# Optimization experiments

Hardware: AMD Instinct MI355X
Metric: run time of the kernel (lower is better)

## Reference

```python
import jax, jax.numpy as jnp
import numpy as np

PRE_NMS_TOPK = 6000
POST_NMS_TOPK = 1000
NMS_THRESH = 0.7
MIN_SIZE = 16.0
NEG = -1e9  # stand-in for -inf that is safe under autodiff


def setup_inputs() -> dict:
    key = jax.random.key(0)
    k1, k2, k3, k4, k5, k6, k7, k8 = jax.random.split(key, 8)
    B, A = 8, 200000
    N = B * A
    # realistic anchors: centers within a ~1333x800 canvas, sizes 16..256
    cx = jax.random.uniform(k1, (N,), minval=0.0, maxval=1200.0)
    cy = jax.random.uniform(k2, (N,), minval=0.0, maxval=800.0)
    w = jax.random.uniform(k3, (N,), minval=16.0, maxval=256.0)
    h = jax.random.uniform(k4, (N,), minval=16.0, maxval=256.0)
    anchors = jnp.stack([cx - 0.5 * w, cy - 0.5 * h, cx + 0.5 * w, cy + 0.5 * h], axis=1)
    batch_indices = jnp.sort(jax.random.randint(k5, (N,), 0, B)).astype(jnp.int32)
    image_sizes = jax.random.randint(k6, (B, 2), 600, 1334).astype(jnp.int32)  # (H, W)
    objectness_logits = jax.random.normal(k7, (N, 1), dtype=jnp.float32)
    bbox_deltas = jax.random.normal(k8, (N, 4), dtype=jnp.float32) * 0.2
    return {
        'anchors': anchors,
        'batch_indices': batch_indices,
        'image_sizes': image_sizes,
        'objectness_logits': objectness_logits,
        'bbox_deltas': bbox_deltas,
    }


def _nms_one(bx, sc):
    """Greedy NMS on [K,4] boxes / [K] scores; returns POST_NMS_TOPK (idx, ok)."""
    K = bx.shape[0]
    areas = (bx[:, 2] - bx[:, 0]) * (bx[:, 3] - bx[:, 1])
    ar = jnp.arange(K)

    def step(sup, _):
        s = jnp.where(sup, NEG, sc)
        j = jnp.argmax(s)
        ok = s[j] > 0.5 * NEG
        b = bx[j]
        ix1 = jnp.maximum(b[0], bx[:, 0])
        iy1 = jnp.maximum(b[1], bx[:, 1])
        ix2 = jnp.minimum(b[2], bx[:, 2])
        iy2 = jnp.minimum(b[3], bx[:, 3])
        inter = jnp.maximum(ix2 - ix1, 0.0) * jnp.maximum(iy2 - iy1, 0.0)
        iou = inter / (areas + areas[j] - inter + 1e-9)
        sup = sup | (iou > NMS_THRESH) | (ar == j)
        return sup, (j, ok)

    sup0 = sc <= 0.5 * NEG  # padded / invalid entries start suppressed
    _, (idx, ok) = jax.lax.scan(step, sup0, None, length=POST_NMS_TOPK)
    return idx, ok


def reference(anchors, batch_indices, image_sizes, objectness_logits, bbox_deltas):
    B = image_sizes.shape[0]
    N = anchors.shape[0]
    sizes = image_sizes[batch_indices].astype(jnp.float32)  # [N,2] (H,W) per anchor

    # --- box decode ---
    a_w = anchors[:, 2] - anchors[:, 0]
    a_h = anchors[:, 3] - anchors[:, 1]
    a_x = anchors[:, 0] + 0.5 * a_w
    a_y = anchors[:, 1] + 0.5 * a_h
    t_x, t_y = bbox_deltas[:, 0], bbox_deltas[:, 1]
    t_w, t_h = bbox_deltas[:, 2], bbox_deltas[:, 3]
    p_x = a_x + t_x * a_w
    p_y = a_y + t_y * a_h
    p_w = a_w * jnp.exp(jnp.clip(t_w, -10.0, 10.0))
    p_h = a_h * jnp.exp(jnp.clip(t_h, -10.0, 10.0))
    x1 = p_x - 0.5 * p_w
    y1 = p_y - 0.5 * p_h
    x2 = p_x + 0.5 * p_w
    y2 = p_y + 0.5 * p_h

    # --- clip to image ---
    H, W = sizes[:, 0], sizes[:, 1]
    x1 = jnp.clip(x1, 0.0, W - 1.0)
    y1 = jnp.clip(y1, 0.0, H - 1.0)
    x2 = jnp.clip(x2, 0.0, W - 1.0)
    y2 = jnp.clip(y2, 0.0, H - 1.0)
    boxes = jnp.stack([x1, y1, x2, y2], axis=1)  # [N,4]

    # --- min-size filter (as score masking) ---
    valid = ((x2 - x1) >= MIN_SIZE) & ((y2 - y1) >= MIN_SIZE)
    fg = jax.nn.sigmoid(objectness_logits[:, 0])

    # --- per-image top-k over masked scores ---
    img_mask = batch_indices[None, :] == jnp.arange(B, dtype=batch_indices.dtype)[:, None]  # [B,N]
    scores = jnp.where(img_mask & valid[None, :], fg[None, :], NEG)  # [B,N]
    top_scores, top_idx = jax.lax.top_k(scores, PRE_NMS_TOPK)  # [B,PRE]
    top_boxes = boxes[top_idx]  # [B,PRE,4]

    # --- NMS per image ---
    keep_idx, keep_ok = jax.vmap(_nms_one)(top_boxes, top_scores)  # [B,POST]

    sel = jnp.take_along_axis(top_idx, keep_idx, axis=1)  # global anchor indices [B,POST]
    okf = keep_ok[..., None].astype(boxes.dtype)
    props = jnp.take_along_axis(top_boxes, keep_idx[..., None], axis=1) * okf  # [B,POST,4]
    obj = objectness_logits[sel] * okf  # [B,POST,1]
    deltas_out = bbox_deltas[sel] * okf  # [B,POST,4]
    bidx = jnp.where(keep_ok, jnp.arange(B, dtype=jnp.int32)[:, None], -1)  # [B,POST]

    return (props.reshape(-1, 4), bidx.reshape(-1), obj.reshape(-1, 1),
            deltas_out.reshape(-1, 4), keep_ok.reshape(-1))
```

## Files before the change

kernel.cpp:

```cpp
#include <hip/hip_runtime.h>
#include <stdint.h>

#define PRE_K   6000
#define POST_K  1000
#define CAP     8192
#define BINS    1024
#define ROWS    6016
#define CH      94
#define JSPLIT  8
#define NEGF    -1000000000.0f
#define IOU_EPS 16.0f
#define KREG    12


__device__ __forceinline__ uint32_t orderf(float f) {
  uint32_t u = __float_as_uint(f);
  return (u & 0x80000000u) ? ~u : (u | 0x80000000u);
}

__device__ __forceinline__ int score_bin(float sc) {
  int bin = (int)floorf((sc + 12.0f) * ((float)BINS / 24.0f));
  return bin < 0 ? 0 : (bin > BINS - 1 ? BINS - 1 : bin);
}

__device__ __forceinline__ int bin_slot(int bin) {
  return ((bin & 15) << 6) | (bin >> 4);
}

__device__ __forceinline__ void wg_barrier_lds() {
  asm volatile("s_waitcnt lgkmcnt(0)" ::: "memory");
  __builtin_amdgcn_s_barrier();
  asm volatile("" ::: "memory");
}

__device__ __forceinline__ void decode_box(
    const float* __restrict__ anchors, const float* __restrict__ deltas,
    const int* __restrict__ isz, int n, int b,
    double& x1, double& y1, double& x2, double& y2, bool& valid) {
  double ax1 = (double)anchors[4 * n + 0], ay1 = (double)anchors[4 * n + 1];
  double ax2 = (double)anchors[4 * n + 2], ay2 = (double)anchors[4 * n + 3];
  double aw = ax2 - ax1, ah = ay2 - ay1;
  double acx = ax1 + 0.5 * aw, acy = ay1 + 0.5 * ah;
  double tx = (double)deltas[4 * n + 0], ty = (double)deltas[4 * n + 1];
  double tw = (double)deltas[4 * n + 2], th = (double)deltas[4 * n + 3];
  tw = tw < -10.0 ? -10.0 : (tw > 10.0 ? 10.0 : tw);
  th = th < -10.0 ? -10.0 : (th > 10.0 ? 10.0 : th);
  double px = acx + tx * aw, py = acy + ty * ah;
  double pw = aw * exp(tw), ph = ah * exp(th);
  double H = (double)isz[2 * b + 0], W = (double)isz[2 * b + 1];
  double wm = W - 1.0, hm = H - 1.0;
  x1 = px - 0.5 * pw; y1 = py - 0.5 * ph;
  x2 = px + 0.5 * pw; y2 = py + 0.5 * ph;
  x1 = fmin(fmax(x1, 0.0), wm); x2 = fmin(fmax(x2, 0.0), wm);
  y1 = fmin(fmax(y1, 0.0), hm); y2 = fmin(fmax(y2, 0.0), hm);
  valid = (x2 - x1 >= 16.0) && (y2 - y1 >= 16.0);
}

__device__ __forceinline__ bool iou_exact(const double* __restrict__ tbox,
                                          const double* __restrict__ tarea,
                                          size_t ri, size_t ci) {
  const double* pr = &tbox[ri * 4];
  const double* pc = &tbox[ci * 4];
  double w = fmin(pr[2], pc[2]) - fmax(pr[0], pc[0]); w = w > 0.0 ? w : 0.0;
  double h = fmin(pr[3], pc[3]) - fmax(pr[1], pc[1]); h = h > 0.0 ? h : 0.0;
  double it = w * h;
  return it > 0.7 * (tarea[ri] + tarea[ci] - it + 1e-9);
}


__global__ void __launch_bounds__(256) k_score(const float* __restrict__ anchors,
                                               const int* __restrict__ bix,
                                               const int* __restrict__ isz,
                                               const float* __restrict__ logits,
                                               const float* __restrict__ deltas,
                                               float* __restrict__ scores,
                                               uint32_t* __restrict__ hist, int N) {
  const int SPAN = 4096;
  int start = blockIdx.x * SPAN;
  int end = start + SPAN < N ? start + SPAN : N;
  __shared__ uint32_t lh[2][BINS];
  for (int i = threadIdx.x; i < 2 * BINS; i += 256) ((uint32_t*)lh)[i] = 0u;
  __shared__ int s_b0, s_b1;
  if (threadIdx.x == 0) { s_b0 = bix[start]; s_b1 = bix[end - 1]; }
  __syncthreads();
  int b0 = s_b0, b1 = s_b1;

  for (int n = start + (int)threadIdx.x; n < end; n += 256) {
    int b = bix[n];
    double x1, y1, x2, y2; bool valid;
    decode_box(anchors, deltas, isz, n, b, x1, y1, x2, y2, valid);
    float sc = valid ? logits[n] : NEGF;
    scores[n] = sc;
    if (valid) {
      int bin = score_bin(sc);
      if (b == b0)      atomicAdd(&lh[0][bin], 1u);
      else if (b == b1) atomicAdd(&lh[1][bin], 1u);
      else              atomicAdd(&hist[b * BINS + bin_slot(bin)], 1u);
    }
  }
  __syncthreads();
  for (int bin = threadIdx.x; bin < BINS; bin += 256) {
    uint32_t c0 = lh[0][bin];
    if (c0) atomicAdd(&hist[b0 * BINS + bin_slot(bin)], c0);
    if (b1 != b0) {
      uint32_t c1 = lh[1][bin];
      if (c1) atomicAdd(&hist[b1 * BINS + bin_slot(bin)], c1);
    }
  }
}

__global__ void __launch_bounds__(1024) k_compact(const float* __restrict__ scores,
                                                  const int* __restrict__ bix,
                                                  const uint32_t* __restrict__ hist,
                                                  uint32_t* __restrict__ cnt,
                                                  uint64_t* __restrict__ cand, int N) {
  const int SPAN = 8192;
  int start = blockIdx.x * SPAN;
  int end = start + SPAN < N ? start + SPAN : N;
  int t = threadIdx.x;
  __shared__ int s_b0, s_b1;
  __shared__ uint32_t sh[BINS];
  __shared__ int s_bs;
  __shared__ uint32_t lcnt[8], lbase[8];
  if (t == 0) { s_b0 = bix[start]; s_b1 = bix[end - 1]; }
  if (t < 8) lcnt[t] = 0u;
  __syncthreads();
  int b0 = s_b0, b1 = s_b1;

  uint32_t bs0 = 0, bs1 = 0;
  for (int pass = 0; pass < 2; pass++) {
    int b = pass == 0 ? b0 : b1;
    if (pass == 1 && b1 == b0) { bs1 = bs0; break; }
    if (t < BINS) sh[t] = hist[b * BINS + bin_slot(t)];
    if (t == 0) s_bs = 0;
    __syncthreads();
    for (int off = 1; off < BINS; off <<= 1) {
      uint32_t v = (t < BINS && t + off < BINS) ? sh[t + off] : 0u;
      __syncthreads();
      if (t < BINS) sh[t] += v;
      __syncthreads();
    }
    if (t < BINS && sh[t] >= PRE_K) atomicMax(&s_bs, t);
    __syncthreads();
    if (pass == 0) bs0 = (uint32_t)s_bs; else bs1 = (uint32_t)s_bs;
    __syncthreads();
  }

  bool     predv[8];
  uint64_t keyv[8];
  uint32_t lposv[8];
  int      bv[8];
  int nt = 0;
  for (int base = start; base < end; base += 1024, nt++) {
    int n = base + t;
    bool pred = false; int b = 0; uint64_t key = 0ull; uint32_t lp = 0u;
    if (n < end) {
      float sc = scores[n];
      if (sc > 0.5f * NEGF) {
        b = bix[n];
        uint32_t bs = (b == b0) ? bs0 : bs1;
        if ((uint32_t)score_bin(sc) >= bs) {
          pred = true;
          key = ((uint64_t)orderf(sc) << 32) | (uint64_t)(uint32_t)(~(uint32_t)n);
          lp = atomicAdd(&lcnt[b], 1u);
        }
      }
    }
    predv[nt] = pred; keyv[nt] = key; lposv[nt] = lp; bv[nt] = b;
  }
  __syncthreads();
  if (t < 8) {
    uint32_t c = lcnt[t];
    lbase[t] = c ? atomicAdd(&cnt[t], c) : 0u;
  }
  __syncthreads();
  for (int k = 0; k < nt; k++) {
    if (predv[k]) {
      uint32_t pos = lbase[bv[k]] + lposv[k];
      if (pos < CAP) cand[(size_t)bv[k] * CAP + pos] = keyv[k];
    }
  }
}

__global__ void __launch_bounds__(256) k_rank(const uint64_t* __restrict__ cand,
                                              const uint32_t* __restrict__ cnt,
                                              uint32_t* __restrict__ prank) {
  int blk = blockIdx.x;
  int js = blk % JSPLIT;
  int ic = (blk / JSPLIT) % 32;
  int b  = blk / (JSPLIT * 32);
  int t = threadIdx.x;
  int C = (int)min(cnt[b], (uint32_t)CAP);
  if (ic * 256 >= C) return;
  const uint64_t* g = cand + (size_t)b * CAP;
  int i = ic * 256 + t;
  uint64_t ki = (i < C) ? g[i] : 0ull;

  int q = (C + JSPLIT - 1) / JSPLIT;
  int j0 = js * q;
  int j1 = j0 + q < C ? j0 + q : C;

  __shared__ uint64_t tile[1024];
  int rank = 0;
  for (int base = j0; base < j1; base += 1024) {
#pragma unroll
    for (int u = 0; u < 4; u++) {
      int j = base + u * 256 + t;
      tile[u * 256 + t] = (j < j1) ? g[j] : 0ull;
    }
    __syncthreads();
    int lim = j1 - base < 1024 ? j1 - base : 1024;
    const ulonglong2* t2 = (const ulonglong2*)tile;
    int pairs = lim >> 1;
    int jj = 0;
    for (; jj + 4 <= pairs; jj += 4) {
      ulonglong2 v0 = t2[jj + 0], v1 = t2[jj + 1];
      ulonglong2 v2 = t2[jj + 2], v3 = t2[jj + 3];
      rank += (v0.x > ki) ? 1 : 0; rank += (v0.y > ki) ? 1 : 0;
      rank += (v1.x > ki) ? 1 : 0; rank += (v1.y > ki) ? 1 : 0;
      rank += (v2.x > ki) ? 1 : 0; rank += (v2.y > ki) ? 1 : 0;
      rank += (v3.x > ki) ? 1 : 0; rank += (v3.y > ki) ? 1 : 0;
    }
    for (; jj < pairs; jj++) {
      ulonglong2 v = t2[jj];
      rank += (v.x > ki) ? 1 : 0; rank += (v.y > ki) ? 1 : 0;
    }
    if (lim & 1) rank += (tile[lim - 1] > ki) ? 1 : 0;
    __syncthreads();
  }
  if (i < C) prank[((size_t)b * JSPLIT + js) * CAP + i] = (uint32_t)rank;
}

__global__ void __launch_bounds__(256) k_place_gather(
    const uint64_t* __restrict__ cand, const uint32_t* __restrict__ cnt,
    const uint32_t* __restrict__ prank,
    const float* __restrict__ anchors, const float* __restrict__ deltas,
    const int* __restrict__ isz,
    double* __restrict__ tbox, double* __restrict__ tarea,
    float4* __restrict__ tboxf, float* __restrict__ tareaf,
    int* __restrict__ top_n, int* __restrict__ Cnum, int B) {
  int idx = blockIdx.x * blockDim.x + threadIdx.x;
  if (idx >= B * CAP) return;
  int b = idx / CAP, i = idx % CAP;
  int C = (int)min(cnt[b], (uint32_t)CAP);
  if (i == 0) Cnum[b] = C < PRE_K ? C : PRE_K;
  if (i >= C) return;
  uint32_t rank = 0;
#pragma unroll
  for (int js = 0; js < JSPLIT; js++)
    rank += prank[((size_t)b * JSPLIT + js) * CAP + i];
  if (rank >= PRE_K) return;
  int n = (int)(~(uint32_t)(cand[idx] & 0xFFFFFFFFull));
  double x1, y1, x2, y2; bool valid;
  decode_box(anchors, deltas, isz, n, b, x1, y1, x2, y2, valid);
  size_t row = (size_t)b * ROWS + rank;
  tbox[row * 4 + 0] = x1;
  tbox[row * 4 + 1] = y1;
  tbox[row * 4 + 2] = x2;
  tbox[row * 4 + 3] = y2;
  double ar = (x2 - x1) * (y2 - y1);
  tarea[row] = ar;
  tboxf[row] = make_float4((float)x1, (float)y1, (float)x2, (float)y2);
  tareaf[row] = (float)ar;
  top_n[b * PRE_K + rank] = n;
}

__global__ void __launch_bounds__(64) k_iou_mat(const float4* __restrict__ tboxf,
                                                const float* __restrict__ tareaf,
                                                const double* __restrict__ tbox,
                                                const double* __restrict__ tarea,
                                                const int* __restrict__ Cnum,
                                                uint32_t* __restrict__ maskT) {
  int rc = blockIdx.x;
  int cc = blockIdx.y;
  int b  = blockIdx.z;
  if (rc > cc) return;
  int C = Cnum[b];
  if (cc * 64 >= C) return;
  int lane = threadIdx.x;
  size_t bb = (size_t)b * ROWS;

  float4 rb4 = tboxf[bb + (size_t)rc * 64 + lane];
  float  sra = 0.7f * tareaf[bb + (size_t)rc * 64 + lane];
  __shared__ float4 cbx[64];
  __shared__ float  csa[64];
  cbx[lane] = tboxf[bb + (size_t)cc * 64 + lane];
  csa[lane] = 0.7f * tareaf[bb + (size_t)cc * 64 + lane];
  __syncthreads();

  bool isdiag = (rc == cc);
  uint32_t res0 = 0u, res1 = 0u;

  for (int j = 0; j < 64; j++) {
    float4 c4 = cbx[j];
    float sca = csa[j];
    float iw = fminf(c4.z, rb4.z) - fmaxf(c4.x, rb4.x);
    float ih = fminf(c4.w, rb4.w) - fmaxf(c4.y, rb4.y);
    iw = fmaxf(iw, 0.0f); ih = fmaxf(ih, 0.0f);
    float inter = iw * ih;
    float diff = fmaf(1.7f, inter, -(sra + sca));
    bool gt = isdiag ? (j > lane) : true;
    bool sup = gt && (diff > IOU_EPS);
    if (gt && !sup && diff > -IOU_EPS) {
      sup = iou_exact(tbox, tarea, bb + (size_t)rc * 64 + lane,
                      bb + (size_t)cc * 64 + j);
    }
    if (sup) { if (j < 32) res0 |= 1u << j; else res1 |= 1u << (j & 31); }
  }
  uint2* seg = (uint2*)(maskT + (((size_t)b * CH + cc) * ROWS + (size_t)rc * 64) * 2);
  seg[lane] = make_uint2(res0, res1);
}

__global__ void __launch_bounds__(256) k_nms_reduce(const uint32_t* __restrict__ maskT,
                                                    const double* __restrict__ tbox,
                                                    const int* __restrict__ Cnum,
                                                    const int* __restrict__ top_n,
                                                    const float* __restrict__ logits,
                                                    const float* __restrict__ deltas,
                                                    float* __restrict__ out, int B) {
  int b = blockIdx.x, t = threadIdx.x;
  int wave = t >> 6, lane = t & 63;
  int C = Cnum[b];
  int nch = (C + 63) >> 6;
  const uint2* Mb = (const uint2*)(maskT + (size_t)b * CH * ROWS * 2);
  size_t bb = (size_t)b * ROWS;

  __shared__ uint32_t acc[CH][2];
  __shared__ uint16_t kept[POST_K];
  __shared__ uint16_t pend[2][64];
  __shared__ int      npend[2];
  __shared__ uint64_t s_kept;

  for (int i = t; i < CH * 2; i += 256) ((uint32_t*)acc)[i] = 0u;
  if (t < 2) npend[t] = 0;
  __syncthreads();

  uint2 dgA = make_uint2(0u,0u), pfA = make_uint2(0u,0u), qfA = make_uint2(0u,0u);
  uint2 dgB = make_uint2(0u,0u), pfB = make_uint2(0u,0u), qfB = make_uint2(0u,0u);
  if (wave == 0) {
    if (nch > 0) {
      dgA = Mb[(size_t)0 * ROWS + 0 + lane];
      if (nch > 1) pfA = Mb[(size_t)1 * ROWS + 0 + lane];
      if (nch > 2) qfA = Mb[(size_t)2 * ROWS + 0 + lane];
    }
    if (nch > 1) {
      dgB = Mb[(size_t)1 * ROWS + 64 + lane];
      if (nch > 2) pfB = Mb[(size_t)2 * ROWS + 64 + lane];
      if (nch > 3) qfB = Mb[(size_t)3 * ROWS + 64 + lane];
    }
  }

  uint2 lz[KREG];
#pragma unroll
  for (int u = 0; u < KREG; u++) lz[u] = make_uint2(0u, 0u);
  int lz_total = 0, lz_cc0 = 0, lz_span = 1;

  int nkept = 0;
  for (int c = 0; c < nch; c++) {
    if (wave == 0) {
      uint2 dgv, pfv, qfv;
      if (c & 1) { dgv = dgB; pfv = pfB; qfv = qfB; }
      else       { dgv = dgA; pfv = pfA; qfv = qfA; }
      int base = c << 6;
      uint64_t sup = (uint64_t)acc[c][0] | ((uint64_t)acc[c][1] << 32);
      int rem = C - base;
      if (rem < 64) sup |= ~((1ull << rem) - 1ull);
      uint64_t diag = (uint64_t)dgv.x | ((uint64_t)dgv.y << 32);
      uint64_t keptMask = 0ull;
      uint64_t alive = ~sup;
      uint64_t m = alive;
      while (m) {
        int i = __builtin_ctzll(m);
        keptMask |= 1ull << i;
        uint64_t d = (uint64_t)__shfl((long long)diag, i, 64);
        sup |= d | (1ull << i);
        m = alive & ~sup;
      }
      int allowed = POST_K - nkept;
      int pc2 = __popcll(keptMask);
      while (pc2 > allowed) {
        keptMask &= ~(1ull << (63 - __builtin_clzll(keptMask)));
        pc2--;
      }
      if (lane == 0) { s_kept = keptMask; npend[c & 1] = pc2; }
      bool mine = (keptMask >> lane) & 1ull;
      if (mine) {
        int pfx = __popcll(keptMask & ((1ull << lane) - 1ull));
        kept[nkept + pfx] = (uint16_t)(base + lane);
        pend[c & 1][pfx] = (uint16_t)(base + lane);
      }
      if (c + 1 < nch) {
        uint32_t v0 = mine ? pfv.x : 0u, v1 = mine ? pfv.y : 0u;
        uint32_t w0 = mine ? qfv.x : 0u, w1 = mine ? qfv.y : 0u;
#pragma unroll
        for (int off = 32; off > 0; off >>= 1) {
          v0 |= (uint32_t)__shfl_xor((int)v0, off, 64);
          v1 |= (uint32_t)__shfl_xor((int)v1, off, 64);
          w0 |= (uint32_t)__shfl_xor((int)w0, off, 64);
          w1 |= (uint32_t)__shfl_xor((int)w1, off, 64);
        }
        if (lane == 0) {
          if (v0) atomicOr(&acc[c + 1][0], v0);
          if (v1) atomicOr(&acc[c + 1][1], v1);
          if (c + 2 < nch) {
            if (w0) atomicOr(&acc[c + 2][0], w0);
            if (w1) atomicOr(&acc[c + 2][1], w1);
          }
        }
      }
      if (c + 2 < nch) {
        int cn = c + 2;
        int nb = cn << 6;
        uint2 d2 = Mb[(size_t)cn * ROWS + nb + lane];
        uint2 p2 = (cn + 1 < nch) ? Mb[(size_t)(cn + 1) * ROWS + nb + lane]
                                  : make_uint2(0u, 0u);
        uint2 q2 = (cn + 2 < nch) ? Mb[(size_t)(cn + 2) * ROWS + nb + lane]
                                  : make_uint2(0u, 0u);
        if (c & 1) { dgB = d2; pfB = p2; qfB = q2; }
        else       { dgA = d2; pfA = p2; qfA = q2; }
      }
    } else {
      if (lz_total > 0) {
#pragma unroll
        for (int u = 0; u < KREG; u++) {
          int it = (t - 64) + u * 192;
          if (it < lz_total) {
            int pi = it / lz_span;
            int cc = lz_cc0 + (it - pi * lz_span);
            if (lz[u].x) atomicOr(&acc[cc][0], lz[u].x);
            if (lz[u].y) atomicOr(&acc[cc][1], lz[u].y);
          }
        }
      }
      int np = (c >= 1) ? npend[(c - 1) & 1] : 0;
      int cc0 = c + 2;
      int span = nch - cc0;
      if (np > 0 && span > 0) {
        int total = np * span;
#pragma unroll
        for (int u = 0; u < KREG; u++) {
          int it = (t - 64) + u * 192;
          uint2 v = make_uint2(0u, 0u);
          if (it < total) {
            int pi = it / span;
            int cc = cc0 + (it - pi * span);
            int row = (int)pend[(c - 1) & 1][pi];
            v = Mb[(size_t)cc * ROWS + row];
          }
          lz[u] = v;
        }
        for (int it = (t - 64) + KREG * 192; it < total; it += 192) {
          int pi = it / span;
          int cc = cc0 + (it - pi * span);
          int row = (int)pend[(c - 1) & 1][pi];
          uint2 v = Mb[(size_t)cc * ROWS + row];
          if (v.x) atomicOr(&acc[cc][0], v.x);
          if (v.y) atomicOr(&acc[cc][1], v.y);
        }
        lz_total = total < KREG * 192 ? total : KREG * 192;
        lz_cc0 = cc0; lz_span = span;
      } else {
        lz_total = 0;
      }
    }
    wg_barrier_lds();

    int pc = __popcll(s_kept);
    nkept += pc;
    if (nkept >= POST_K) break;
  }

  __syncthreads();
  int M_out = B * POST_K;
  for (int s2 = t; s2 < POST_K; s2 += 256) {
    float p0 = 0.f, p1 = 0.f, p2 = 0.f, p3 = 0.f;
    float ob = 0.f, d0f = 0.f, d1f = 0.f, d2f = 0.f, d3f = 0.f;
    float bi = -1.0f, okv = 0.0f;
    if (s2 < nkept) {
      int j = (int)kept[s2];
      int n = top_n[b * PRE_K + j];
      const double* p = &tbox[(bb + j) * 4];
      p0 = (float)p[0]; p1 = (float)p[1]; p2 = (float)p[2]; p3 = (float)p[3];
      ob = logits[n];
      d0f = deltas[4 * n + 0]; d1f = deltas[4 * n + 1];
      d2f = deltas[4 * n + 2]; d3f = deltas[4 * n + 3];
      bi = (float)b; okv = 1.0f;
    }
    int idx = b * POST_K + s2;
    out[idx * 4 + 0] = p0;
    out[idx * 4 + 1] = p1;
    out[idx * 4 + 2] = p2;
    out[idx * 4 + 3] = p3;
    out[4 * M_out + idx] = bi;
    out[5 * M_out + idx] = ob;
    out[6 * M_out + idx * 4 + 0] = d0f;
    out[6 * M_out + idx * 4 + 1] = d1f;
    out[6 * M_out + idx * 4 + 2] = d2f;
    out[6 * M_out + idx * 4 + 3] = d3f;
    out[10 * M_out + idx] = okv;
  }
}


extern "C" void kernel_launch(void* const* d_in, const int* in_sizes, int n_in,
                              void* d_out, int out_size, void* d_ws, size_t ws_size,
                              hipStream_t stream) {
  const float* anchors = (const float*)d_in[0];
  const int*   bix     = (const int*)d_in[1];
  const int*   isz     = (const int*)d_in[2];
  const float* logits  = (const float*)d_in[3];
  const float* deltas  = (const float*)d_in[4];
  float* out = (float*)d_out;

  int N = in_sizes[1];
  int B = in_sizes[2] / 2;

  uintptr_t p = (uintptr_t)d_ws;
  double*   tbox   = (double*)p;    p += (size_t)B * ROWS * 4 * sizeof(double);
  double*   tarea  = (double*)p;    p += (size_t)B * ROWS * sizeof(double);
  uint64_t* cand   = (uint64_t*)p;  p += (size_t)B * CAP * sizeof(uint64_t);
  float*    scores = (float*)p;     p += (size_t)N * sizeof(float);
  uint32_t* hist   = (uint32_t*)p;  p += (size_t)B * BINS * sizeof(uint32_t);
  uint32_t* cnt    = (uint32_t*)p;  p += (size_t)B * sizeof(uint32_t);
  uint32_t* prank  = (uint32_t*)p;  p += (size_t)B * JSPLIT * CAP * sizeof(uint32_t);
  int*      top_n    = (int*)p;     p += (size_t)B * PRE_K * sizeof(int);
  int*      Cnum     = (int*)p;      p += (size_t)B * sizeof(int);
  p = (p + 255) & ~(uintptr_t)255;
  uint32_t* maskT    = (uint32_t*)p; p += (size_t)B * CH * ROWS * 2 * sizeof(uint32_t);
  float4*   tboxf  = (float4*)scores;
  float*    tareaf = (float*)(scores + (size_t)B * ROWS * 4);
  (void)ws_size; (void)n_in; (void)out_size;

  hipMemsetAsync(hist, 0, (size_t)(B * BINS + B) * sizeof(uint32_t), stream);
  k_score<<<(N + 4095) / 4096, 256, 0, stream>>>(anchors, bix, isz, logits, deltas,
                                                 scores, hist, N);
  k_compact<<<(N + 8191) / 8192, 1024, 0, stream>>>(scores, bix, hist, cnt, cand, N);
  k_rank<<<B * 32 * JSPLIT, 256, 0, stream>>>(cand, cnt, prank);
  k_place_gather<<<(B * CAP + 255) / 256, 256, 0, stream>>>(cand, cnt, prank,
                                                            anchors, deltas, isz,
                                                            tbox, tarea, tboxf,
                                                            tareaf, top_n, Cnum, B);
  dim3 iou_grid(CH, CH, B);
  k_iou_mat<<<iou_grid, 64, 0, stream>>>(tboxf, tareaf, tbox, tarea, Cnum, maskT);
  k_nms_reduce<<<B, 256, 0, stream>>>(maskT, tbox, Cnum, top_n, logits, deltas,
                                      out, B);
}
```

Baseline: 384.2 us.

## Deepen NMS mask pipeline to three chunks ahead with double-buffered lazy ORs

The serial NMS scan wave now prefetches and ORs suppression rows for three following chunks instead of two, and the helper waves defer their global-row ORs by two iterations using A/B register buffers. The goal is to give the global mask loads more time to arrive before they are needed. Cross-lane broadcasts now use readlane/readfirstlane instead of shfl, and the butterfly OR reduction is replaced by a loop over kept lanes. This raises register pressure, since there are twice as many lz registers plus an extra prefetch set, and it adds scalar work that scales with the number of kept boxes.

```diff
diff --git a/kernel.cpp b/kernel.cpp
--- a/kernel.cpp
+++ b/kernel.cpp
@@ -31,6 +31,10 @@
   asm volatile("s_waitcnt lgkmcnt(0)" ::: "memory");
   __builtin_amdgcn_s_barrier();
   asm volatile("" ::: "memory");
+}
+
+__device__ __forceinline__ uint32_t rdlane(uint32_t v, int i) {
+  return (uint32_t)__builtin_amdgcn_readlane((int)v, i);
 }
 
 __device__ __forceinline__ void decode_box(
@@ -335,44 +339,51 @@
   if (t < 2) npend[t] = 0;
   __syncthreads();
 
-  uint2 dgA = make_uint2(0u,0u), pfA = make_uint2(0u,0u), qfA = make_uint2(0u,0u);
-  uint2 dgB = make_uint2(0u,0u), pfB = make_uint2(0u,0u), qfB = make_uint2(0u,0u);
+  uint2 dgA = make_uint2(0u,0u), pfA = make_uint2(0u,0u),
+        qfA = make_uint2(0u,0u), rfA = make_uint2(0u,0u);
+  uint2 dgB = make_uint2(0u,0u), pfB = make_uint2(0u,0u),
+        qfB = make_uint2(0u,0u), rfB = make_uint2(0u,0u);
   if (wave == 0) {
     if (nch > 0) {
       dgA = Mb[(size_t)0 * ROWS + 0 + lane];
       if (nch > 1) pfA = Mb[(size_t)1 * ROWS + 0 + lane];
       if (nch > 2) qfA = Mb[(size_t)2 * ROWS + 0 + lane];
+      if (nch > 3) rfA = Mb[(size_t)3 * ROWS + 0 + lane];
     }
     if (nch > 1) {
       dgB = Mb[(size_t)1 * ROWS + 64 + lane];
       if (nch > 2) pfB = Mb[(size_t)2 * ROWS + 64 + lane];
       if (nch > 3) qfB = Mb[(size_t)3 * ROWS + 64 + lane];
-    }
-  }
-
-  uint2 lz[KREG];
-#pragma unroll
-  for (int u = 0; u < KREG; u++) lz[u] = make_uint2(0u, 0u);
-  int lz_total = 0, lz_cc0 = 0, lz_span = 1;
+      if (nch > 4) rfB = Mb[(size_t)4 * ROWS + 64 + lane];
+    }
+  }
+
+  uint2 lzA[KREG], lzB[KREG];
+#pragma unroll
+  for (int u = 0; u < KREG; u++) { lzA[u] = make_uint2(0u,0u); lzB[u] = make_uint2(0u,0u); }
+  int mA_total = 0, mA_cc0 = 0, mA_span = 1;
+  int mB_total = 0, mB_cc0 = 0, mB_span = 1;
 
   int nkept = 0;
   for (int c = 0; c < nch; c++) {
     if (wave == 0) {
-      uint2 dgv, pfv, qfv;
-      if (c & 1) { dgv = dgB; pfv = pfB; qfv = qfB; }
-      else       { dgv = dgA; pfv = pfA; qfv = qfA; }
+      uint2 dgv, pfv, qfv, rfv;
+      if (c & 1) { dgv = dgB; pfv = pfB; qfv = qfB; rfv = rfB; }
+      else       { dgv = dgA; pfv = pfA; qfv = qfA; rfv = rfA; }
       int base = c << 6;
-      uint64_t sup = (uint64_t)acc[c][0] | ((uint64_t)acc[c][1] << 32);
+      uint32_t a0 = (uint32_t)__builtin_amdgcn_readfirstlane((int)acc[c][0]);
+      uint32_t a1 = (uint32_t)__builtin_amdgcn_readfirstlane((int)acc[c][1]);
+      uint64_t sup = (uint64_t)a0 | ((uint64_t)a1 << 32);
       int rem = C - base;
       if (rem < 64) sup |= ~((1ull << rem) - 1ull);
-      uint64_t diag = (uint64_t)dgv.x | ((uint64_t)dgv.y << 32);
       uint64_t keptMask = 0ull;
       uint64_t alive = ~sup;
       uint64_t m = alive;
       while (m) {
         int i = __builtin_ctzll(m);
         keptMask |= 1ull << i;
-        uint64_t d = (uint64_t)__shfl((long long)diag, i, 64);
+        uint64_t d = (uint64_t)rdlane(dgv.x, i)
+                   | ((uint64_t)rdlane(dgv.y, i) << 32);
         sup |= d | (1ull << i);
         m = alive & ~sup;
       }
@@ -389,15 +400,15 @@
         kept[nkept + pfx] = (uint16_t)(base + lane);
         pend[c & 1][pfx] = (uint16_t)(base + lane);
       }
-      if (c + 1 < nch) {
-        uint32_t v0 = mine ? pfv.x : 0u, v1 = mine ? pfv.y : 0u;
-        uint32_t w0 = mine ? qfv.x : 0u, w1 = mine ? qfv.y : 0u;
-#pragma unroll
-        for (int off = 32; off > 0; off >>= 1) {
-          v0 |= (uint32_t)__shfl_xor((int)v0, off, 64);
-          v1 |= (uint32_t)__shfl_xor((int)v1, off, 64);
-          w0 |= (uint32_t)__shfl_xor((int)w0, off, 64);
-          w1 |= (uint32_t)__shfl_xor((int)w1, off, 64);
+      if (c + 1 < nch && keptMask) {
+        uint32_t v0 = 0u, v1 = 0u, w0 = 0u, w1 = 0u, x0 = 0u, x1 = 0u;
+        uint64_t km = keptMask;
+        while (km) {
+          int i = __builtin_ctzll(km);
+          km &= km - 1ull;
+          v0 |= rdlane(pfv.x, i); v1 |= rdlane(pfv.y, i);
+          w0 |= rdlane(qfv.x, i); w1 |= rdlane(qfv.y, i);
+          x0 |= rdlane(rfv.x, i); x1 |= rdlane(rfv.y, i);
         }
         if (lane == 0) {
           if (v0) atomicOr(&acc[c + 1][0], v0);
@@ -405,6 +416,10 @@
           if (c + 2 < nch) {
             if (w0) atomicOr(&acc[c + 2][0], w0);
             if (w1) atomicOr(&acc[c + 2][1], w1);
+          }
+          if (c + 3 < nch) {
+            if (x0) atomicOr(&acc[c + 3][0], x0);
+            if (x1) atomicOr(&acc[c + 3][1], x1);
           }
         }
       }
@@ -416,38 +431,73 @@
                                   : make_uint2(0u, 0u);
         uint2 q2 = (cn + 2 < nch) ? Mb[(size_t)(cn + 2) * ROWS + nb + lane]
                                   : make_uint2(0u, 0u);
-        if (c & 1) { dgB = d2; pfB = p2; qfB = q2; }
-        else       { dgA = d2; pfA = p2; qfA = q2; }
+        uint2 r2 = (cn + 3 < nch) ? Mb[(size_t)(cn + 3) * ROWS + nb + lane]
+                                  : make_uint2(0u, 0u);
+        if (c & 1) { dgB = d2; pfB = p2; qfB = q2; rfB = r2; }
+        else       { dgA = d2; pfA = p2; qfA = q2; rfA = r2; }
       }
     } else {
-      if (lz_total > 0) {
-#pragma unroll
-        for (int u = 0; u < KREG; u++) {
-          int it = (t - 64) + u * 192;
-          if (it < lz_total) {
-            int pi = it / lz_span;
-            int cc = lz_cc0 + (it - pi * lz_span);
-            if (lz[u].x) atomicOr(&acc[cc][0], lz[u].x);
-            if (lz[u].y) atomicOr(&acc[cc][1], lz[u].y);
+      if (c & 1) {
+        if (mB_total > 0) {
+#pragma unroll
+          for (int u = 0; u < KREG; u++) {
+            int it = (t - 64) + u * 192;
+            if (it < mB_total) {
+              int pi = it / mB_span;
+              int cc = mB_cc0 + (it - pi * mB_span);
+              if (lzB[u].x) atomicOr(&acc[cc][0], lzB[u].x);
+              if (lzB[u].y) atomicOr(&acc[cc][1], lzB[u].y);
+            }
           }
         }
+      } else {
+        if (mA_total > 0) {
+#pragma unroll
+          for (int u = 0; u < KREG; u++) {
+            int it = (t - 64) + u * 192;
+            if (it < mA_total) {
+              int pi = it / mA_span;
+              int cc = mA_cc0 + (it - pi * mA_span);
+              if (lzA[u].x) atomicOr(&acc[cc][0], lzA[u].x);
+              if (lzA[u].y) atomicOr(&acc[cc][1], lzA[u].y);
+            }
+          }
+        }
       }
       int np = (c >= 1) ? npend[(c - 1) & 1] : 0;
-      int cc0 = c + 2;
+      int cc0 = c + 3;
       int span = nch - cc0;
-      if (np > 0 && span > 0) {
-        int total = np * span;
-#pragma unroll
-        for (int u = 0; u < KREG; u++) {
-          int it = (t - 64) + u * 192;
-          uint2 v = make_uint2(0u, 0u);
-          if (it < total) {
-            int pi = it / span;
-            int cc = cc0 + (it - pi * span);
-            int row = (int)pend[(c - 1) & 1][pi];
-            v = Mb[(size_t)cc * ROWS + row];
+      int total = (np > 0 && span > 0) ? np * span : 0;
+      if (total > 0) {
+        int capn = total < KREG * 192 ? total : KREG * 192;
+        if (c & 1) {
+#pragma unroll
+          for (int u = 0; u < KREG; u++) {
+            int it = (t - 64) + u * 192;
+            uint2 v = make_uint2(0u, 0u);
+            if (it < total) {
+              int pi = it / span;
+              int cc = cc0 + (it - pi * span);
+              int row = (int)pend[(c - 1) & 1][pi];
+              v = Mb[(size_t)cc * ROWS + row];
+            }
+            lzB[u] = v;
           }
-          lz[u] = v;
+          mB_total = capn; mB_cc0 = cc0; mB_span = span;
+        } else {
+#pragma unroll
+          for (int u = 0; u < KREG; u++) {
+            int it = (t - 64) + u * 192;
+            uint2 v = make_uint2(0u, 0u);
+            if (it < total) {
+              int pi = it / span;
+              int cc = cc0 + (it - pi * span);
+              int row = (int)pend[(c - 1) & 1][pi];
+              v = Mb[(size_t)cc * ROWS + row];
+            }
+            lzA[u] = v;
+          }
+          mA_total = capn; mA_cc0 = cc0; mA_span = span;
         }
         for (int it = (t - 64) + KREG * 192; it < total; it += 192) {
           int pi = it / span;
@@ -457,10 +507,8 @@
           if (v.x) atomicOr(&acc[cc][0], v.x);
           if (v.y) atomicOr(&acc[cc][1], v.y);
         }
-        lz_total = total < KREG * 192 ? total : KREG * 192;
-        lz_cc0 = cc0; lz_span = span;
       } else {
-        lz_total = 0;
+        if (c & 1) mB_total = 0; else mA_total = 0;
       }
     }
     wg_barrier_lds();
```

Measured after the change: 395.0 us. 1.03x slower.

## Run NMS reduce loop in single wave, dropping per-chunk workgroup barriers

Applied to the files above, without the earlier changes.

The sequential NMS reduction loop now runs entirely in wave 0. The lazy propagation of suppression rows into later chunks moves from the other three waves into wave 0 itself, using double-buffered register arrays (KREG raised to 16). This removes one workgroup barrier per 64-box chunk, which sat on the serial critical path. In exchange, one wave now does all the global mask loads and LDS atomics, so chunks with many kept boxes may take longer per iteration.

```diff
diff --git a/kernel.cpp b/kernel.cpp
--- a/kernel.cpp
+++ b/kernel.cpp
@@ -10,7 +10,7 @@
 #define JSPLIT  8
 #define NEGF    -1000000000.0f
 #define IOU_EPS 16.0f
-#define KREG    12
+#define KREG    16
 
 
 __device__ __forceinline__ uint32_t orderf(float f) {
@@ -25,12 +25,6 @@
 
 __device__ __forceinline__ int bin_slot(int bin) {
   return ((bin & 15) << 6) | (bin >> 4);
-}
-
-__device__ __forceinline__ void wg_barrier_lds() {
-  asm volatile("s_waitcnt lgkmcnt(0)" ::: "memory");
-  __builtin_amdgcn_s_barrier();
-  asm volatile("" ::: "memory");
 }
 
 __device__ __forceinline__ void decode_box(
@@ -327,42 +321,59 @@
 
   __shared__ uint32_t acc[CH][2];
   __shared__ uint16_t kept[POST_K];
-  __shared__ uint16_t pend[2][64];
-  __shared__ int      npend[2];
-  __shared__ uint64_t s_kept;
+  __shared__ uint16_t pend[64];
+  __shared__ int      s_nkept;
 
   for (int i = t; i < CH * 2; i += 256) ((uint32_t*)acc)[i] = 0u;
-  if (t < 2) npend[t] = 0;
-  __syncthreads();
-
-  uint2 dgA = make_uint2(0u,0u), pfA = make_uint2(0u,0u), qfA = make_uint2(0u,0u);
-  uint2 dgB = make_uint2(0u,0u), pfB = make_uint2(0u,0u), qfB = make_uint2(0u,0u);
-  if (wave == 0) {
-    if (nch > 0) {
-      dgA = Mb[(size_t)0 * ROWS + 0 + lane];
-      if (nch > 1) pfA = Mb[(size_t)1 * ROWS + 0 + lane];
-      if (nch > 2) qfA = Mb[(size_t)2 * ROWS + 0 + lane];
-    }
-    if (nch > 1) {
-      dgB = Mb[(size_t)1 * ROWS + 64 + lane];
-      if (nch > 2) pfB = Mb[(size_t)2 * ROWS + 64 + lane];
-      if (nch > 3) qfB = Mb[(size_t)3 * ROWS + 64 + lane];
-    }
-  }
-
-  uint2 lz[KREG];
-#pragma unroll
-  for (int u = 0; u < KREG; u++) lz[u] = make_uint2(0u, 0u);
-  int lz_total = 0, lz_cc0 = 0, lz_span = 1;
-
-  int nkept = 0;
-  for (int c = 0; c < nch; c++) {
-    if (wave == 0) {
+  if (t == 0) s_nkept = 0;
+  __syncthreads();
+
+  if (wave == 0 && nch > 0) {
+    const uint2 z2 = make_uint2(0u, 0u);
+    uint2 dgA = Mb[(size_t)0 * ROWS + lane];
+    uint2 pfA = (nch > 1) ? Mb[(size_t)1 * ROWS + lane] : z2;
+    uint2 qfA = (nch > 2) ? Mb[(size_t)2 * ROWS + lane] : z2;
+    uint2 dgB = (nch > 1) ? Mb[(size_t)1 * ROWS + 64 + lane] : z2;
+    uint2 pfB = (nch > 2) ? Mb[(size_t)2 * ROWS + 64 + lane] : z2;
+    uint2 qfB = (nch > 3) ? Mb[(size_t)3 * ROWS + 64 + lane] : z2;
+
+    uint2 lzA[KREG], lzB[KREG];
+#pragma unroll
+    for (int u = 0; u < KREG; u++) { lzA[u] = z2; lzB[u] = z2; }
+    int nA = 0, ccA = 0, spA = 0;
+    int nB = 0, ccB = 0, spB = 0;
+
+    uint32_t pa0 = 0u, pa1 = 0u;
+    int nkept = 0;
+
+    for (int c = 0; c < nch; c++) {
+      if (c & 1) {
+        if (nB > 0) {
+#pragma unroll
+          for (int u = 0; u < KREG; u++) {
+            if (u < nB && lane < spB) {
+              if (lzB[u].x) atomicOr(&acc[ccB + lane][0], lzB[u].x);
+              if (lzB[u].y) atomicOr(&acc[ccB + lane][1], lzB[u].y);
+            }
+          }
+        }
+      } else {
+        if (nA > 0) {
+#pragma unroll
+          for (int u = 0; u < KREG; u++) {
+            if (u < nA && lane < spA) {
+              if (lzA[u].x) atomicOr(&acc[ccA + lane][0], lzA[u].x);
+              if (lzA[u].y) atomicOr(&acc[ccA + lane][1], lzA[u].y);
+            }
+          }
+        }
+      }
+
       uint2 dgv, pfv, qfv;
       if (c & 1) { dgv = dgB; pfv = pfB; qfv = qfB; }
       else       { dgv = dgA; pfv = pfA; qfv = qfA; }
       int base = c << 6;
-      uint64_t sup = (uint64_t)acc[c][0] | ((uint64_t)acc[c][1] << 32);
+      uint64_t sup = (uint64_t)pa0 | ((uint64_t)pa1 << 32);
       int rem = C - base;
       if (rem < 64) sup |= ~((1ull << rem) - 1ull);
       uint64_t diag = (uint64_t)dgv.x | ((uint64_t)dgv.y << 32);
@@ -382,14 +393,15 @@
         keptMask &= ~(1ull << (63 - __builtin_clzll(keptMask)));
         pc2--;
       }
-      if (lane == 0) { s_kept = keptMask; npend[c & 1] = pc2; }
       bool mine = (keptMask >> lane) & 1ull;
       if (mine) {
         int pfx = __popcll(keptMask & ((1ull << lane) - 1ull));
         kept[nkept + pfx] = (uint16_t)(base + lane);
-        pend[c & 1][pfx] = (uint16_t)(base + lane);
-      }
-      if (c + 1 < nch) {
+        pend[pfx] = (uint16_t)(base + lane);
+      }
+      nkept += pc2;
+
+      if (c + 1 < nch && keptMask) {
         uint32_t v0 = mine ? pfv.x : 0u, v1 = mine ? pfv.y : 0u;
         uint32_t w0 = mine ? qfv.x : 0u, w1 = mine ? qfv.y : 0u;
 #pragma unroll
@@ -408,69 +420,67 @@
           }
         }
       }
+
       if (c + 2 < nch) {
         int cn = c + 2;
         int nb = cn << 6;
         uint2 d2 = Mb[(size_t)cn * ROWS + nb + lane];
-        uint2 p2 = (cn + 1 < nch) ? Mb[(size_t)(cn + 1) * ROWS + nb + lane]
-                                  : make_uint2(0u, 0u);
-        uint2 q2 = (cn + 2 < nch) ? Mb[(size_t)(cn + 2) * ROWS + nb + lane]
-                                  : make_uint2(0u, 0u);
+        uint2 p2 = (cn + 1 < nch) ? Mb[(size_t)(cn + 1) * ROWS + nb + lane] : z2;
+        uint2 q2 = (cn + 2 < nch) ? Mb[(size_t)(cn + 2) * ROWS + nb + lane] : z2;
         if (c & 1) { dgB = d2; pfB = p2; qfB = q2; }
         else       { dgA = d2; pfA = p2; qfA = q2; }
       }
-    } else {
-      if (lz_total > 0) {
-#pragma unroll
-        for (int u = 0; u < KREG; u++) {
-          int it = (t - 64) + u * 192;
-          if (it < lz_total) {
-            int pi = it / lz_span;
-            int cc = lz_cc0 + (it - pi * lz_span);
-            if (lz[u].x) atomicOr(&acc[cc][0], lz[u].x);
-            if (lz[u].y) atomicOr(&acc[cc][1], lz[u].y);
+
+      {
+        int cc0 = c + 3;
+        int span = nch - cc0;
+        if (span < 0) span = 0;
+        int npi = (span > 0) ? pc2 : 0;
+        int rowv = (npi > 0) ? (int)pend[lane] : 0;
+        int cap = npi < KREG ? npi : KREG;
+        if (c & 1) {
+#pragma unroll
+          for (int u = 0; u < KREG; u++) {
+            uint2 v = z2;
+            if (u < cap) {
+              int row = __shfl(rowv, u, 64);
+              if (lane < span) v = Mb[(size_t)(cc0 + lane) * ROWS + row];
+            }
+            lzB[u] = v;
           }
-        }
-      }
-      int np = (c >= 1) ? npend[(c - 1) & 1] : 0;
-      int cc0 = c + 2;
-      int span = nch - cc0;
-      if (np > 0 && span > 0) {
-        int total = np * span;
-#pragma unroll
-        for (int u = 0; u < KREG; u++) {
-          int it = (t - 64) + u * 192;
-          uint2 v = make_uint2(0u, 0u);
-          if (it < total) {
-            int pi = it / span;
-            int cc = cc0 + (it - pi * span);
-            int row = (int)pend[(c - 1) & 1][pi];
-            v = Mb[(size_t)cc * ROWS + row];
+          nB = cap; ccB = cc0; spB = span;
+        } else {
+#pragma unroll
+          for (int u = 0; u < KREG; u++) {
+            uint2 v = z2;
+            if (u < cap) {
+              int row = __shfl(rowv, u, 64);
+              if (lane < span) v = Mb[(size_t)(cc0 + lane) * ROWS + row];
+            }
+            lzA[u] = v;
           }
-          lz[u] = v;
-        }
-        for (int it = (t - 64) + KREG * 192; it < total; it += 192) {
-          int pi = it / span;
-          int cc = cc0 + (it - pi * span);
-          int row = (int)pend[(c - 1) & 1][pi];
-          uint2 v = Mb[(size_t)cc * ROWS + row];
-          if (v.x) atomicOr(&acc[cc][0], v.x);
-          if (v.y) atomicOr(&acc[cc][1], v.y);
-        }
-        lz_total = total < KREG * 192 ? total : KREG * 192;
-        lz_cc0 = cc0; lz_span = span;
-      } else {
-        lz_total = 0;
-      }
-    }
-    wg_barrier_lds();
-
-    int pc = __popcll(s_kept);
-    nkept += pc;
-    if (nkept >= POST_K) break;
-  }
-
-  __syncthreads();
+          nA = cap; ccA = cc0; spA = span;
+        }
+        for (int u = KREG; u < npi; u++) {
+          int row = __shfl(rowv, u, 64);
+          if (lane < span) {
+            uint2 v = Mb[(size_t)(cc0 + lane) * ROWS + row];
+            if (v.x) atomicOr(&acc[cc0 + lane][0], v.x);
+            if (v.y) atomicOr(&acc[cc0 + lane][1], v.y);
+          }
+        }
+      }
+
+      pa0 = 0u; pa1 = 0u;
+      if (c + 1 < nch) { pa0 = acc[c + 1][0]; pa1 = acc[c + 1][1]; }
+
+      if (nkept >= POST_K) break;
+    }
+    if (lane == 0) s_nkept = nkept;
+  }
+  __syncthreads();
+
+  int nkept = s_nkept;
   int M_out = B * POST_K;
   for (int s2 = t; s2 < POST_K; s2 += 256) {
     float p0 = 0.f, p1 = 0.f, p2 = 0.f, p3 = 0.f;
```

Measured after the change: 536.9 us. +39.8%, slower.
